# Performance work log

Hardware: AMD Instinct MI355X
Metric: run time of the kernel (lower is better)

## Reference

```python
import jax, jax.numpy as jnp
import numpy as np

S, B, E, H = 512, 64, 256, 256


def _cell(h, c, xt, wih, whh, bih, bhh):
    # PyTorch LSTM gate order: i, f, g, o
    z = xt @ wih.T + h @ whh.T + bih + bhh  # (B, 4H)
    i, f, g, o = jnp.split(z, 4, axis=-1)
    c = jax.nn.sigmoid(f) * c + jax.nn.sigmoid(i) * jnp.tanh(g)
    h = jax.nn.sigmoid(o) * jnp.tanh(c)
    return h, c


def _bilstm(x, h0, c0, wih_f, whh_f, bih_f, bhh_f, wih_b, whh_b, bih_b, bhh_b):
    # x: (T,B,E); h0,c0: (2,B,H) -> out (T,B,2H), hn/cn (2,B,H)
    def fstep(carry, xt):
        h, c = _cell(carry[0], carry[1], xt, wih_f, whh_f, bih_f, bhh_f)
        return (h, c), h

    def bstep(carry, xt):
        h, c = _cell(carry[0], carry[1], xt, wih_b, whh_b, bih_b, bhh_b)
        return (h, c), h

    (hf, cf), out_f = jax.lax.scan(fstep, (h0[0], c0[0]), x)
    (hb, cb), out_b_rev = jax.lax.scan(bstep, (h0[1], c0[1]), x[::-1])
    out = jnp.concatenate([out_f, out_b_rev[::-1]], axis=-1)
    return out, jnp.stack([hf, hb]), jnp.stack([cf, cb])


def setup_inputs() -> dict:
    key = jax.random.key(0)
    ks = jax.random.split(key, 9)
    s = 1.0 / np.sqrt(H)
    u = lambda k, shape: jax.random.uniform(k, shape, jnp.float32, -s, s)
    return {
        "inputs": jax.random.normal(ks[0], (S, B, E), jnp.float32),
        "wih_f": u(ks[1], (4 * H, E)), "whh_f": u(ks[2], (4 * H, H)),
        "bih_f": u(ks[3], (4 * H,)), "bhh_f": u(ks[4], (4 * H,)),
        "wih_b": u(ks[5], (4 * H, E)), "whh_b": u(ks[6], (4 * H, H)),
        "bih_b": u(ks[7], (4 * H,)), "bhh_b": u(ks[8], (4 * H,)),
    }


def reference(inputs, wih_f, whh_f, bih_f, bhh_f, wih_b, whh_b, bih_b, bhh_b):
    seq, batch = inputs.shape[0], inputs.shape[1]
    params = (wih_f, whh_f, bih_f, bhh_f, wih_b, whh_b, bih_b, bhh_b)
    # windows i=0..S-2 are each 2 tokens: inputs[i:i+2]
    windows = jnp.stack([inputs[:-1], inputs[1:]], axis=1)  # (S-1, 2, B, E)

    def step(carry, win):
        h, c = carry
        out, hn, cn = _bilstm(win, h, c, *params)
        return (hn, cn), out  # out (2,B,2H)

    h0 = jnp.zeros((2, batch, H), inputs.dtype)
    c0 = jnp.zeros((2, batch, H), inputs.dtype)
    (hl, cl), outs = jax.lax.scan(step, (h0, c0), windows)
    # final window i=S-1 is length 1, seeded with the state from window S-2
    out_last, _, _ = _bilstm(inputs[-1:], hl, cl, *params)  # (1,B,2H)
    hidden = jnp.concatenate(
        [outs.reshape(2 * (seq - 1), batch, 2 * H), out_last], axis=0
    )  # (2S-1, B, 2H)
    # AdaptiveMaxPool1d(1) over the time axis
    emb = hidden.max(axis=0)  # (B, 2H)
    return emb
```

## Files before the change

kernel.cpp:

```cpp
#include <hip/hip_runtime.h>

typedef __attribute__((ext_vector_type(8))) short short8;
typedef __attribute__((ext_vector_type(4))) float f32x4;
typedef __attribute__((ext_vector_type(4))) unsigned short u16x4;
typedef __attribute__((ext_vector_type(4))) unsigned int u32x4;

#define S_ 512
#define B_ 64
#define E_ 256
#define H_ 256
#define NSTEP 1023

__device__ __forceinline__ unsigned short f2bf(float f) {
  unsigned u = __builtin_bit_cast(unsigned, f);
  return (unsigned short)((u + 0x7fffu + ((u >> 16) & 1u)) >> 16);
}
__device__ __forceinline__ float bf2f(unsigned short h) {
  unsigned u = ((unsigned)h) << 16;
  return __builtin_bit_cast(float, u);
}
__device__ __forceinline__ float sigm(float x) { return 1.f / (1.f + __expf(-x)); }
__device__ __forceinline__ float tanh_(float x) {
  x = fminf(fmaxf(x, -15.f), 15.f);
  float e = __expf(-2.f * x);
  return (1.f - e) / (1.f + e);
}

__global__ __launch_bounds__(256) void prep9(
    const float* __restrict__ x,
    const float* __restrict__ wih_f, const float* __restrict__ whh_f,
    const float* __restrict__ bih_f, const float* __restrict__ bhh_f,
    const float* __restrict__ wih_b, const float* __restrict__ whh_b,
    const float* __restrict__ bih_b, const float* __restrict__ bhh_b,
    short* __restrict__ x_bf, short* __restrict__ wx, short* __restrict__ wh,
    float* __restrict__ bias_p)
{
  long i0 = (long)blockIdx.x * blockDim.x + threadIdx.x;
  long stride = (long)gridDim.x * blockDim.x;
  const long NX = (long)S_ * B_ * E_;
  const long NW = 2L * 1024 * 256;
  const long NB = 2L * 1024;

  for (long i = i0; i < NX; i += stride) x_bf[i] = (short)f2bf(x[i]);

  for (long i = i0; i < NW; i += stride) {
    int ch  = (int)(i >> 18);
    int rem = (int)(i & 262143);
    int p   = rem >> 8;
    int k   = rem & 255;
    int jc  = p >> 2, g = p & 3;
    long j  = (long)(g * 256 + jc);
    wx[i] = (short)f2bf((ch ? wih_b : wih_f)[j * 256 + k]);
    wh[i] = (short)f2bf((ch ? whh_b : whh_f)[j * 256 + k]);
  }

  for (long i = i0; i < NB; i += stride) {
    int ch = (int)(i >> 10);
    int p  = (int)(i & 1023);
    int jc = p >> 2, g = p & 3;
    int j  = g * 256 + jc;
    bias_p[i] = ch ? (bih_b[j] + bhh_b[j]) : (bih_f[j] + bhh_f[j]);
  }
}

__global__ __launch_bounds__(512, 2) void xz_gemm9(
    const short* __restrict__ x_bf, const short* __restrict__ wx,
    const float* __restrict__ bias_p, short* __restrict__ xz)
{
  const int bid = blockIdx.x;
  const int ch = bid >> 9, t = bid & 511;
  const int tid = threadIdx.x;
  const int wave = tid >> 6, lane = tid & 63;
  const int l15 = lane & 15, l4 = lane >> 4;

  const short* W = wx + (long)ch * 1024 * 256;
  const short* X = x_bf + (long)t * B_ * E_;

  f32x4 acc[8][4];
#pragma unroll
  for (int mt = 0; mt < 8; ++mt)
#pragma unroll
    for (int nt = 0; nt < 4; ++nt) acc[mt][nt] = (f32x4){0.f, 0.f, 0.f, 0.f};

#pragma unroll
  for (int ks = 0; ks < 8; ++ks) {
    int k0 = ks * 32 + l4 * 8;
    short8 bfr[4];
#pragma unroll
    for (int nt = 0; nt < 4; ++nt)
      bfr[nt] = *(const short8*)(X + (long)(nt * 16 + l15) * E_ + k0);
#pragma unroll
    for (int mt = 0; mt < 8; ++mt) {
      int p = (wave * 8 + mt) * 16 + l15;
      short8 af = *(const short8*)(W + (long)p * 256 + k0);
#pragma unroll
      for (int nt = 0; nt < 4; ++nt)
        acc[mt][nt] = __builtin_amdgcn_mfma_f32_16x16x32_bf16(af, bfr[nt], acc[mt][nt], 0, 0, 0);
    }
  }

#pragma unroll
  for (int mt = 0; mt < 8; ++mt) {
    int jc = (wave * 8 + mt) * 4 + l4;
    f32x4 b4 = *(const f32x4*)(bias_p + ch * 1024 + jc * 4);
#pragma unroll
    for (int nt = 0; nt < 4; ++nt) {
      int b = nt * 16 + l15;
      u16x4 v;
#pragma unroll
      for (int g = 0; g < 4; ++g) v[g] = f2bf(acc[mt][nt][g] + b4[g]);
      long off = (((long)(ch * 512 + t) * 256 + jc) * 64 + b) * 4;
      *(u16x4*)(xz + off) = v;
    }
  }
}

__global__ __launch_bounds__(512) void lstm12(
    const short* __restrict__ wh, const short* __restrict__ xz,
    short* __restrict__ hring, float* __restrict__ out)
{
  const int bid  = blockIdx.x;
  const int ch   = bid >> 4;
  const int bs   = (bid >> 2) & 3;
  const int role = bid & 3;
  const int tid  = threadIdx.x;
  const int wave = tid >> 6, lane = tid & 63;
  const int l15 = lane & 15, l4 = lane >> 4;

  __shared__ short hin[2][16 * 256];

  for (int i = tid; i < 2 * 16 * 256; i += 512) ((short*)hin)[i] = 0;

  const short* whc = wh + (long)ch * 1024 * 256;

  short8 ah[2][8];
#pragma unroll
  for (int mt = 0; mt < 2; ++mt)
#pragma unroll
    for (int ks = 0; ks < 8; ++ks)
      ah[mt][ks] = *(const short8*)(whc + (long)(role * 256 + wave * 32 + mt * 16 + l15) * 256 + ks * 32 + l4 * 8);

  float cst[2], hmax[2];
#pragma unroll
  for (int mt = 0; mt < 2; ++mt) { cst[mt] = 0.f; hmax[mt] = -2.f; }

  short* rb = hring + ch * 16384;
  const int swzr = (l15 & 7) << 4;

  const int sb = tid >> 4, sc = tid & 15;
  const int pb = tid >> 5, pc = tid & 31;
  const int own = (pc >> 3) == role;

  __syncthreads();

  for (int t = 0; t < NSTEP; ++t) {
    int tok;
    if (ch == 0) tok = (t + 1) >> 1;
    else         tok = (t == NSTEP - 1) ? (S_ - 1) : ((t & 1) ? (t >> 1) : (t >> 1) + 1);

    u16x4 xq[2];
#pragma unroll
    for (int mt = 0; mt < 2; ++mt) {
      int jc = role * 64 + wave * 8 + mt * 4 + l4;
      long off = (((long)(ch * 512 + tok) * 256 + jc) * 64 + (bs * 16 + l15)) * 4;
      xq[mt] = *(const u16x4*)(xz + off);
    }

    if (tid < 256) {
      short* pa = rb + ((t + 1) & 3) * 32768 + (bs * 16 + sb) * 256 + role * 64 + sc * 4;
      unsigned long long pv = 0xFFFFFFFFFFFFFFFFull;
      asm volatile("global_store_dwordx2 %0, %1, off sc1" :: "v"(pa), "v"(pv) : "memory");
    }

    {
      const short* ga = rb + ((t + 3) & 3) * 32768 + (bs * 16 + pb) * 256 + pc * 8;
      short8 hv;
      int bad;
      do {
        bad = 0;
        if (!own) {
          asm volatile("global_load_dwordx4 %0, %1, off sc1\n\ts_waitcnt vmcnt(0)"
                       : "=v"(hv) : "v"(ga) : "memory");
          u32x4 dv = __builtin_bit_cast(u32x4, hv);
#pragma unroll
          for (int i = 0; i < 4; ++i) {
            unsigned d = dv[i];
            bad |= ((d & 0xFFFFu) == 0xFFFFu) | ((d >> 16) == 0xFFFFu);
          }
        }
      } while (__ballot(bad));
      if (!own)
        *(short8*)((char*)hin[t & 1] + pb * 512 + ((pc * 16) ^ ((pb & 7) << 4))) = hv;
    }
    __syncthreads();

    f32x4 acc[2];
    acc[0] = (f32x4){0.f, 0.f, 0.f, 0.f};
    acc[1] = (f32x4){0.f, 0.f, 0.f, 0.f};
    const char* hr = (const char*)hin[t & 1] + l15 * 512;
#pragma unroll
    for (int ks = 0; ks < 8; ++ks) {
      short8 hfr = *(const short8*)(hr + ((ks * 64 + l4 * 16) ^ swzr));
      acc[0] = __builtin_amdgcn_mfma_f32_16x16x32_bf16(ah[0][ks], hfr, acc[0], 0, 0, 0);
      acc[1] = __builtin_amdgcn_mfma_f32_16x16x32_bf16(ah[1][ks], hfr, acc[1], 0, 0, 0);
    }

    short* rslot = rb + (t & 3) * 32768 + (bs * 16 + l15) * 256;
    char* hnext = (char*)hin[(t + 1) & 1] + l15 * 512;
#pragma unroll
    for (int mt = 0; mt < 2; ++mt) {
      float zi = acc[mt][0] + bf2f(xq[mt][0]);
      float zf = acc[mt][1] + bf2f(xq[mt][1]);
      float zg = acc[mt][2] + bf2f(xq[mt][2]);
      float zo = acc[mt][3] + bf2f(xq[mt][3]);
      float cc = cst[mt];
      cc = sigm(zf) * cc + sigm(zi) * tanh_(zg);
      float hh = sigm(zo) * tanh_(cc);
      cst[mt] = cc;
      hmax[mt] = fmaxf(hmax[mt], hh);
      unsigned short hb = f2bf(hh);
      int col = role * 64 + wave * 8 + mt * 4 + l4;
      *(short*)(hnext + ((col * 2) ^ swzr)) = (short)hb;
      unsigned hv32 = (unsigned)hb;
      short* ga = rslot + col;
      asm volatile("global_store_short %0, %1, off sc1" :: "v"(ga), "v"(hv32) : "memory");
    }
  }

#pragma unroll
  for (int mt = 0; mt < 2; ++mt) {
    int jc = role * 64 + wave * 8 + mt * 4 + l4;
    out[(long)(bs * 16 + l15) * (2 * H_) + ch * H_ + jc] = hmax[mt];
  }
}

extern "C" void kernel_launch(void* const* d_in, const int* in_sizes, int n_in,
                              void* d_out, int out_size, void* d_ws, size_t ws_size,
                              hipStream_t stream) {
  const float* x     = (const float*)d_in[0];
  const float* wih_f = (const float*)d_in[1];
  const float* whh_f = (const float*)d_in[2];
  const float* bih_f = (const float*)d_in[3];
  const float* bhh_f = (const float*)d_in[4];
  const float* wih_b = (const float*)d_in[5];
  const float* whh_b = (const float*)d_in[6];
  const float* bih_b = (const float*)d_in[7];
  const float* bhh_b = (const float*)d_in[8];

  char* ws = (char*)d_ws;
  short* x_bf   = (short*)(ws);
  short* hring  = (short*)(ws);
  short* wx     = (short*)(ws + 16777216);
  short* wh     = (short*)(ws + 17825792);
  float* bias_p = (float*)(ws + 18874368);
  short* xz     = (short*)(ws + 18882560);

  const size_t NEED = 18882560UL + 134217728UL;
  if (ws_size < NEED) return;

  prep9<<<2048, 256, 0, stream>>>(x, wih_f, whh_f, bih_f, bhh_f,
                                  wih_b, whh_b, bih_b, bhh_b,
                                  x_bf, wx, wh, bias_p);
  xz_gemm9<<<1024, 512, 0, stream>>>(x_bf, wx, bias_p, xz);

  hipMemsetAsync(ws, 0xFF, 196608, stream);
  hipMemsetAsync(ws + 196608, 0, 65536, stream);

  lstm12<<<32, 512, 0, stream>>>(wh, xz, hring, (float*)d_out);
}
```

Measured before the change: 2.099 ms.

## Process both LSTM directions in one block with LDS-resident backward weights

The recurrent kernel now launches 16 blocks instead of 32. Each block handles both direction chains for its batch slice and role, holding forward recurrent weights in registers and backward weights in a 128KB swizzled LDS buffer. The h-exchange ring is re-laid out column-major per direction and batch slice, and every thread now polls its columns. The two chains are interleaved so one chain's global spin-wait latency can overlap with the other's compute. In exchange, each block does twice the serial work per step, adds extra barriers, and reads weights from LDS, which could lengthen the critical path.

```diff
diff --git a/kernel.cpp b/kernel.cpp
--- a/kernel.cpp
+++ b/kernel.cpp
@@ -115,122 +115,161 @@
   }
 }
 
-__global__ __launch_bounds__(512) void lstm12(
+__global__ __launch_bounds__(512) void lstm13(
     const short* __restrict__ wh, const short* __restrict__ xz,
-    short* __restrict__ hring, float* __restrict__ out)
+    short* __restrict__ ring, float* __restrict__ out)
 {
   const int bid  = blockIdx.x;
-  const int ch   = bid >> 4;
-  const int bs   = (bid >> 2) & 3;
+  const int bs   = bid >> 2;
   const int role = bid & 3;
   const int tid  = threadIdx.x;
   const int wave = tid >> 6, lane = tid & 63;
   const int l15 = lane & 15, l4 = lane >> 4;
 
-  __shared__ short hin[2][16 * 256];
-
-  for (int i = tid; i < 2 * 16 * 256; i += 512) ((short*)hin)[i] = 0;
-
-  const short* whc = wh + (long)ch * 1024 * 256;
-
-  short8 ah[2][8];
+  __shared__ short wB[256 * 256];
+  __shared__ short hinA[16 * 256];
+  __shared__ short hinB[16 * 256];
+
+  const short* whA = wh;
+  const short* whB = wh + 1024 * 256;
+
+  {
+    char* wl = (char*)wB;
+#pragma unroll
+    for (int c = 0; c < 16; ++c) {
+      int chunk = c * 512 + tid;
+      int row = chunk >> 5;
+      int c16 = chunk & 31;
+      short8 v = *(const short8*)(whB + (long)(role * 256 + row) * 256 + c16 * 8);
+      *(short8*)(wl + row * 512 + ((c16 * 16) ^ ((row & 7) << 4))) = v;
+    }
+    for (int i = tid; i < 16 * 256; i += 512) { hinA[i] = 0; hinB[i] = 0; }
+  }
+
+  short8 ahA[2][8];
 #pragma unroll
   for (int mt = 0; mt < 2; ++mt)
 #pragma unroll
     for (int ks = 0; ks < 8; ++ks)
-      ah[mt][ks] = *(const short8*)(whc + (long)(role * 256 + wave * 32 + mt * 16 + l15) * 256 + ks * 32 + l4 * 8);
-
-  float cst[2], hmax[2];
-#pragma unroll
-  for (int mt = 0; mt < 2; ++mt) { cst[mt] = 0.f; hmax[mt] = -2.f; }
-
-  short* rb = hring + ch * 16384;
+      ahA[mt][ks] = *(const short8*)(whA + (long)(role * 256 + wave * 32 + mt * 16 + l15) * 256 + ks * 32 + l4 * 8);
+
+  float cstA[2], hmA[2], cstB[2], hmB[2];
+#pragma unroll
+  for (int mt = 0; mt < 2; ++mt) { cstA[mt] = 0.f; hmA[mt] = -2.f; cstB[mt] = 0.f; hmB[mt] = -2.f; }
+
   const int swzr = (l15 & 7) << 4;
-
-  const int sb = tid >> 4, sc = tid & 15;
-  const int pb = tid >> 5, pc = tid & 31;
-  const int own = (pc >> 3) == role;
+  const int colIdx = tid >> 1, halfT = tid & 1;
+  const int rcol = colIdx + ((colIdx >= role * 64) ? 64 : 0);
+  const int active = tid < 384;
+  const int wBbase = (wave * 32 + l15) * 512;
 
   __syncthreads();
 
   for (int t = 0; t < NSTEP; ++t) {
-    int tok;
-    if (ch == 0) tok = (t + 1) >> 1;
-    else         tok = (t == NSTEP - 1) ? (S_ - 1) : ((t & 1) ? (t >> 1) : (t >> 1) + 1);
-
-    u16x4 xq[2];
-#pragma unroll
-    for (int mt = 0; mt < 2; ++mt) {
-      int jc = role * 64 + wave * 8 + mt * 4 + l4;
-      long off = (((long)(ch * 512 + tok) * 256 + jc) * 64 + (bs * 16 + l15)) * 4;
-      xq[mt] = *(const u16x4*)(xz + off);
-    }
-
-    if (tid < 256) {
-      short* pa = rb + ((t + 1) & 3) * 32768 + (bs * 16 + sb) * 256 + role * 64 + sc * 4;
-      unsigned long long pv = 0xFFFFFFFFFFFFFFFFull;
-      asm volatile("global_store_dwordx2 %0, %1, off sc1" :: "v"(pa), "v"(pv) : "memory");
-    }
-
-    {
-      const short* ga = rb + ((t + 3) & 3) * 32768 + (bs * 16 + pb) * 256 + pc * 8;
-      short8 hv;
-      int bad;
-      do {
-        bad = 0;
-        if (!own) {
+    const int slotP = ((t + 1) & 3), slotR = ((t + 3) & 3), slotW = (t & 3);
+
+#pragma unroll
+    for (int cc = 0; cc < 2; ++cc) {
+      int tok;
+      if (cc == 0) tok = (t + 1) >> 1;
+      else         tok = (t == NSTEP - 1) ? (S_ - 1) : ((t & 1) ? (t >> 1) : (t >> 1) + 1);
+      short* hinX = cc ? hinB : hinA;
+
+      short* rP = ring + ((slotP * 2 + cc) * 4 + bs) * 4096;
+      short* rR = ring + ((slotR * 2 + cc) * 4 + bs) * 4096;
+      short* rW = ring + ((slotW * 2 + cc) * 4 + bs) * 4096;
+
+      u16x4 xq[2];
+#pragma unroll
+      for (int mt = 0; mt < 2; ++mt) {
+        int jc = role * 64 + wave * 8 + mt * 4 + l4;
+        long off = (((long)(cc * 512 + tok) * 256 + jc) * 64 + (bs * 16 + l15)) * 4;
+        xq[mt] = *(const u16x4*)(xz + off);
+      }
+
+      if (tid < 256) {
+        short* pa = rP + role * 1024 + tid * 4;
+        unsigned long long pv = 0xFFFFFFFFFFFFFFFFull;
+        asm volatile("global_store_dwordx2 %0, %1, off sc1" :: "v"(pa), "v"(pv) : "memory");
+      }
+
+      if (active) {
+        const short* ga = rR + rcol * 16 + halfT * 8;
+        short8 hv;
+        int bad;
+        do {
           asm volatile("global_load_dwordx4 %0, %1, off sc1\n\ts_waitcnt vmcnt(0)"
                        : "=v"(hv) : "v"(ga) : "memory");
           u32x4 dv = __builtin_bit_cast(u32x4, hv);
+          bad = 0;
 #pragma unroll
           for (int i = 0; i < 4; ++i) {
             unsigned d = dv[i];
             bad |= ((d & 0xFFFFu) == 0xFFFFu) | ((d >> 16) == 0xFFFFu);
           }
+        } while (__ballot(bad));
+#pragma unroll
+        for (int j = 0; j < 8; ++j) {
+          int row = halfT * 8 + j;
+          *(short*)((char*)hinX + row * 512 + ((rcol * 2) ^ (j << 4))) = hv[j];
         }
-      } while (__ballot(bad));
-      if (!own)
-        *(short8*)((char*)hin[t & 1] + pb * 512 + ((pc * 16) ^ ((pb & 7) << 4))) = hv;
-    }
-    __syncthreads();
-
-    f32x4 acc[2];
-    acc[0] = (f32x4){0.f, 0.f, 0.f, 0.f};
-    acc[1] = (f32x4){0.f, 0.f, 0.f, 0.f};
-    const char* hr = (const char*)hin[t & 1] + l15 * 512;
-#pragma unroll
-    for (int ks = 0; ks < 8; ++ks) {
-      short8 hfr = *(const short8*)(hr + ((ks * 64 + l4 * 16) ^ swzr));
-      acc[0] = __builtin_amdgcn_mfma_f32_16x16x32_bf16(ah[0][ks], hfr, acc[0], 0, 0, 0);
-      acc[1] = __builtin_amdgcn_mfma_f32_16x16x32_bf16(ah[1][ks], hfr, acc[1], 0, 0, 0);
-    }
-
-    short* rslot = rb + (t & 3) * 32768 + (bs * 16 + l15) * 256;
-    char* hnext = (char*)hin[(t + 1) & 1] + l15 * 512;
-#pragma unroll
-    for (int mt = 0; mt < 2; ++mt) {
-      float zi = acc[mt][0] + bf2f(xq[mt][0]);
-      float zf = acc[mt][1] + bf2f(xq[mt][1]);
-      float zg = acc[mt][2] + bf2f(xq[mt][2]);
-      float zo = acc[mt][3] + bf2f(xq[mt][3]);
-      float cc = cst[mt];
-      cc = sigm(zf) * cc + sigm(zi) * tanh_(zg);
-      float hh = sigm(zo) * tanh_(cc);
-      cst[mt] = cc;
-      hmax[mt] = fmaxf(hmax[mt], hh);
-      unsigned short hb = f2bf(hh);
-      int col = role * 64 + wave * 8 + mt * 4 + l4;
-      *(short*)(hnext + ((col * 2) ^ swzr)) = (short)hb;
-      unsigned hv32 = (unsigned)hb;
-      short* ga = rslot + col;
-      asm volatile("global_store_short %0, %1, off sc1" :: "v"(ga), "v"(hv32) : "memory");
+      }
+      __syncthreads();
+
+      f32x4 acc[2];
+      acc[0] = (f32x4){0.f, 0.f, 0.f, 0.f};
+      acc[1] = (f32x4){0.f, 0.f, 0.f, 0.f};
+      const char* hr = (const char*)hinX + l15 * 512;
+      if (cc == 0) {
+#pragma unroll
+        for (int ks = 0; ks < 8; ++ks) {
+          short8 hfr = *(const short8*)(hr + ((ks * 64 + l4 * 16) ^ swzr));
+          acc[0] = __builtin_amdgcn_mfma_f32_16x16x32_bf16(ahA[0][ks], hfr, acc[0], 0, 0, 0);
+          acc[1] = __builtin_amdgcn_mfma_f32_16x16x32_bf16(ahA[1][ks], hfr, acc[1], 0, 0, 0);
+        }
+      } else {
+        const char* wl = (const char*)wB;
+#pragma unroll
+        for (int ks = 0; ks < 8; ++ks) {
+          int koff = (ks * 64 + l4 * 16) ^ swzr;
+          short8 hfr = *(const short8*)(hr + koff);
+          short8 w0 = *(const short8*)(wl + wBbase + koff);
+          short8 w1 = *(const short8*)(wl + wBbase + 8192 + koff);
+          acc[0] = __builtin_amdgcn_mfma_f32_16x16x32_bf16(w0, hfr, acc[0], 0, 0, 0);
+          acc[1] = __builtin_amdgcn_mfma_f32_16x16x32_bf16(w1, hfr, acc[1], 0, 0, 0);
+        }
+      }
+      __syncthreads();
+
+      float* cst = cc ? cstB : cstA;
+      float* hm  = cc ? hmB  : hmA;
+#pragma unroll
+      for (int mt = 0; mt < 2; ++mt) {
+        float zi = acc[mt][0] + bf2f(xq[mt][0]);
+        float zf = acc[mt][1] + bf2f(xq[mt][1]);
+        float zg = acc[mt][2] + bf2f(xq[mt][2]);
+        float zo = acc[mt][3] + bf2f(xq[mt][3]);
+        float cv = cst[mt];
+        cv = sigm(zf) * cv + sigm(zi) * tanh_(zg);
+        float hh = sigm(zo) * tanh_(cv);
+        cst[mt] = cv;
+        hm[mt] = fmaxf(hm[mt], hh);
+        unsigned short hb = f2bf(hh);
+        int col = role * 64 + wave * 8 + mt * 4 + l4;
+        *(short*)((char*)hinX + l15 * 512 + ((col * 2) ^ swzr)) = (short)hb;
+        unsigned hv32 = (unsigned)hb;
+        short* ga = rW + col * 16 + l15;
+        asm volatile("global_store_short %0, %1, off sc1" :: "v"(ga), "v"(hv32) : "memory");
+      }
     }
   }
 
 #pragma unroll
   for (int mt = 0; mt < 2; ++mt) {
     int jc = role * 64 + wave * 8 + mt * 4 + l4;
-    out[(long)(bs * 16 + l15) * (2 * H_) + ch * H_ + jc] = hmax[mt];
+    long rowb = (long)(bs * 16 + l15) * (2 * H_);
+    out[rowb + jc] = hmA[mt];
+    out[rowb + H_ + jc] = hmB[mt];
   }
 }
 
@@ -249,7 +288,7 @@
 
   char* ws = (char*)d_ws;
   short* x_bf   = (short*)(ws);
-  short* hring  = (short*)(ws);
+  short* ring   = (short*)(ws);
   short* wx     = (short*)(ws + 16777216);
   short* wh     = (short*)(ws + 17825792);
   float* bias_p = (float*)(ws + 18874368);
@@ -266,5 +305,5 @@
   hipMemsetAsync(ws, 0xFF, 196608, stream);
   hipMemsetAsync(ws + 196608, 0, 65536, stream);
 
-  lstm12<<<32, 512, 0, stream>>>(wh, xz, hring, (float*)d_out);
-}
+  lstm13<<<16, 512, 0, stream>>>(wh, xz, ring, (float*)d_out);
+}
```

Result: slower. 3.804 ms (+81.3%).
